# Optimization experiments

Hardware: AMD Instinct MI355X
Metric: run time of the kernel (lower is better)

The kernel has to match this reference:

```python
import jax, jax.numpy as jnp
import numpy as np
from jax import lax

RO = 4.0            # snake_config.ro (feature-map downsample ratio)
N_ADJ = 4           # snake_config.adj_num -> kernel = 2*4+1 = 9
K = 2 * N_ADJ + 1
DIL = (1, 1, 1, 2, 2, 4, 4)   # dilations of the 7 Snake residual circular convs
NMS_RADIUS = 2      # radius used in the iterative refinement cls_nms


def circ_conv(x, w, b, d):
    """Dilated circular conv along polygon axis. x:[N,C,P], w:[O,I,K]."""
    pad = N_ADJ * d
    xp = jnp.concatenate([x[..., -pad:], x, x[..., :pad]], axis=-1)
    y = lax.conv_general_dilated(xp, w, window_strides=(1,), padding='VALID',
                                 rhs_dilation=(d,),
                                 dimension_numbers=('NCH', 'OIH', 'NCH'))
    return y + b[None, :, None]


def conv1x1(x, w, b):
    # x:[N,C,P], w:[O,C] -> [N,O,P]
    return jnp.einsum('ncp,oc->nop', x, w) + b[None, :, None]


def bilinear_gather(cnn_feature, poly, ind):
    """grid_sample-style bilinear sampling (align_corners=False, zero pad).
    cnn_feature:[B,C,H,W], poly:[N,P,2] pixel coords, ind:[N] image index.
    Returns [N,C,P]."""
    B, C, H, W = cnn_feature.shape
    x = poly[..., 0] - 0.5
    y = poly[..., 1] - 0.5
    x0 = jnp.floor(x); y0 = jnp.floor(y)
    wx = x - x0; wy = y - y0
    x0i = x0.astype(jnp.int32); y0i = y0.astype(jnp.int32)

    def tap(yi, xi):
        valid = (xi >= 0) & (xi < W) & (yi >= 0) & (yi < H)
        xi_c = jnp.clip(xi, 0, W - 1)
        yi_c = jnp.clip(yi, 0, H - 1)
        f = cnn_feature[ind[:, None], :, yi_c, xi_c]  # [N,P,C]
        return f * valid[..., None]

    f00 = tap(y0i, x0i);     f01 = tap(y0i, x0i + 1)
    f10 = tap(y0i + 1, x0i); f11 = tap(y0i + 1, x0i + 1)
    out = (f00 * ((1 - wx) * (1 - wy))[..., None]
           + f01 * (wx * (1 - wy))[..., None]
           + f10 * ((1 - wx) * wy)[..., None]
           + f11 * (wx * wy)[..., None])
    return out.transpose(0, 2, 1)  # [N,C,P]


def cls_nms(cls, radius):
    """Circular local-max suppression of per-vertex scores. cls:[N,P,1]."""
    c = cls[..., 0]
    m = jnp.max(jnp.stack([jnp.roll(c, s, axis=1)
                           for s in range(-radius, radius + 1)], 0), axis=0)
    return jnp.where(c >= m, c, 0.0)[..., None]


def snake_body(x, head_w, head_b, res_w, res_b, fusion_w, fusion_b,
               pred1_w, pred1_b, pred2_w, pred2_b, pred3_w, pred3_b,
               cls1_w, cls1_b, cls2_w, cls2_b, cls3_w, cls3_b):
    h = jax.nn.relu(circ_conv(x, head_w, head_b, 1))
    states = [h]
    for i in range(7):  # fixed 7 residual layers, structurally distinct dilations
        r = jax.nn.relu(circ_conv(states[-1], res_w[i], res_b[i], DIL[i]))
        states.append(r + states[-1])
    state = jnp.concatenate(states, axis=1)                 # [N, 8*128, P]
    g = conv1x1(state, fusion_w, fusion_b)                  # [N, 256, P]
    g = jnp.max(g, axis=2, keepdims=True)
    g = jnp.broadcast_to(g, (state.shape[0], g.shape[1], state.shape[2]))
    state = jnp.concatenate([g, state], axis=1)             # [N, 1280, P]

    def head3(w1, b1, w2, b2, w3, b3):
        h1 = jax.nn.relu(conv1x1(state, w1, b1))
        h2 = jax.nn.relu(conv1x1(h1, w2, b2))
        return conv1x1(h2, w3, b3)

    offset = head3(pred1_w, pred1_b, pred2_w, pred2_b, pred3_w, pred3_b)  # [N,2,P]
    cls = head3(cls1_w, cls1_b, cls2_w, cls2_b, cls3_w, cls3_b)           # [N,1,P]
    return offset, cls


def setup_inputs() -> dict:
    key = jax.random.key(0)
    ks = jax.random.split(key, 32)
    B, C, H, W = 4, 64, 128, 128
    N, P = 512, 128
    SD = 128  # state_dim
    FD = 64 + 2 + 1  # feature_dim for iterative evolve_gcn
    std = 0.01  # conv init: normal(0, 0.01), bias 0 (matches module init)
    inp = {
        'cnn_feature': jax.random.normal(ks[0], (B, C, H, W), jnp.float32),
        'i_it_py': jax.random.uniform(ks[1], (N, P, 2), jnp.float32) * (W - 1),
        'c_it_py': jax.random.normal(ks[2], (N, P, 2), jnp.float32) * 0.2,
        'it_cls': jax.random.uniform(ks[3], (N, P), jnp.float32),
        'ind': jax.random.randint(ks[4], (N,), 0, B, jnp.int32),
        'head_w': jax.random.normal(ks[5], (SD, FD, K), jnp.float32) * std,
        'head_b': jnp.zeros((SD,), jnp.float32),
        'res_w': jax.random.normal(ks[6], (7, SD, SD, K), jnp.float32) * std,
        'res_b': jnp.zeros((7, SD), jnp.float32),
        'fusion_w': jax.random.normal(ks[7], (256, 8 * SD), jnp.float32) * std,
        'fusion_b': jnp.zeros((256,), jnp.float32),
        'pred1_w': jax.random.normal(ks[8], (256, 8 * SD + 256), jnp.float32) * std,
        'pred1_b': jnp.zeros((256,), jnp.float32),
        'pred2_w': jax.random.normal(ks[9], (64, 256), jnp.float32) * std,
        'pred2_b': jnp.zeros((64,), jnp.float32),
        'pred3_w': jax.random.normal(ks[10], (2, 64), jnp.float32) * std,
        'pred3_b': jnp.zeros((2,), jnp.float32),
        'cls1_w': jax.random.normal(ks[11], (256, 8 * SD + 256), jnp.float32) * std,
        'cls1_b': jnp.zeros((256,), jnp.float32),
        'cls2_w': jax.random.normal(ks[12], (64, 256), jnp.float32) * std,
        'cls2_b': jnp.zeros((64,), jnp.float32),
        'cls3_w': jax.random.normal(ks[13], (1, 64), jnp.float32) * std,
        'cls3_b': jnp.zeros((1,), jnp.float32),
    }
    return inp


def reference(cnn_feature, i_it_py, c_it_py, it_cls, ind,
              head_w, head_b, res_w, res_b, fusion_w, fusion_b,
              pred1_w, pred1_b, pred2_w, pred2_b, pred3_w, pred3_b,
              cls1_w, cls1_b, cls2_w, cls2_b, cls3_w, cls3_b):
    # evolve_poly: gather CNN features at vertices, concat scaled canonical
    # coords + per-vertex cls, run Snake, add offsets, NMS sigmoid scores.
    feat = bilinear_gather(cnn_feature, i_it_py, ind)        # [N,64,P]
    c = (c_it_py * RO).transpose(0, 2, 1)                    # [N,2,P]
    x = jnp.concatenate([feat, c, it_cls[:, None, :]], axis=1)  # [N,67,P]
    offset, cls = snake_body(x, head_w, head_b, res_w, res_b, fusion_w, fusion_b,
                             pred1_w, pred1_b, pred2_w, pred2_b, pred3_w, pred3_b,
                             cls1_w, cls1_b, cls2_w, cls2_b, cls3_w, cls3_b)
    i_poly = i_it_py * RO + offset.transpose(0, 2, 1)        # [N,P,2]
    cls = cls.transpose(0, 2, 1)                             # [N,P,1]
    nms = cls_nms(jax.nn.sigmoid(cls), NMS_RADIUS)           # [N,P,1]
    return i_poly, cls, nms
```

## Files before the change

kernel.cpp:

```cpp
#include <hip/hip_runtime.h>
#include <math.h>

typedef __attribute__((ext_vector_type(8))) short bf16x8;
typedef __attribute__((ext_vector_type(4))) float f32x4;

#define UOFF_CAW 0L
#define UOFF_FAW 2359296L
#define UOFF_H1W 2883584L
#define NB_TOT   3932160L
#define OFF_W1G  1966080L
#define OFF_W2S  2097152L
#define OFF_GRAW 2129920L
#define OFF_HG   2260992L
#define OFF_DYN  2523136L
#define REPACK_N 4096000L

__device__ inline ushort f2bf_rne(float x) {
  uint u = __float_as_uint(x);
  return (ushort)((u + 0x7FFFu + ((u >> 16) & 1u)) >> 16);
}
__device__ inline void split_bf(float x, ushort& h, ushort& l) {
  uint u = __float_as_uint(x);
  uint hb = (u + 0x7FFFu + ((u >> 16) & 1u)) & 0xFFFF0000u;
  h = (ushort)(hb >> 16);
  l = f2bf_rne(x - __uint_as_float(hb));
}
__device__ inline ushort bfsel(float w, int split) {
  uint u = __float_as_uint(w);
  uint hb = (u + 0x7FFFu + ((u >> 16) & 1u)) & 0xFFFF0000u;
  if (split == 0) return (ushort)(hb >> 16);
  float lo = w - __uint_as_float(hb);
  uint ul = __float_as_uint(lo);
  return (ushort)((ul + 0x7FFFu + ((ul >> 16) & 1u)) >> 16);
}
__device__ inline bf16x8 asb(uint4 a) {
  union { uint4 u; bf16x8 v; } x; x.u = a; return x.v;
}
__device__ inline f32x4 MFMA_(bf16x8 a, bf16x8 b, f32x4 c) {
  return __builtin_amdgcn_mfma_f32_16x16x32_bf16(a, b, c, 0, 0, 0);
}
__device__ inline uint2 pack2(ushort a, ushort b, ushort c, ushort d) {
  return make_uint2((uint)a | ((uint)b << 16), (uint)c | ((uint)d << 16));
}
__device__ inline void bar_lgkm() {
  asm volatile("s_waitcnt lgkmcnt(0)" ::: "memory");
  __builtin_amdgcn_s_barrier();
}

__device__ inline void read_frag_pair(const char* xb, int pc, int g, int ic,
                                      bf16x8& bh, bf16x8& bl) {
  const int s0 = (pc & 7) << 4;
  const char* a = xb + pc * 512 + (((ic * 64 + (g << 4))) ^ s0);
  bh = asb(*(const uint4*)a);
  bl = asb(*(const uint4*)(a + 256));
}

__global__ void k_repack(const float* __restrict__ head_w, const float* __restrict__ res_w,
                         const float* __restrict__ fusion_w,
                         const float* __restrict__ pred1_w, const float* __restrict__ cls1_w,
                         const float* __restrict__ pred2_w, const float* __restrict__ cls2_w,
                         float* __restrict__ ws) {
  const long j = (long)blockIdx.x * 256 + threadIdx.x;
  if (j >= REPACK_N) return;
  if (j < NB_TOT) {
    ushort* wsu = (ushort*)ws;
    float w;
    if (j < UOFF_FAW) {
      int e = (int)(j & 7); long q = j >> 3;
      int lane = (int)(q & 63); q >>= 6;
      int mt = (int)(q & 1); q >>= 1;
      int split = (int)(q & 1); q >>= 1;
      int ic = (int)(q & 3); q >>= 2;
      int tap = (int)(q % 9); q /= 9;
      int mp = (int)(q & 3); int l = (int)(q >> 2);
      int gg = lane >> 4;
      int kl = (e < 4) ? (4 * gg + e) : (16 + 4 * gg + e - 4);
      int m = mp * 32 + mt * 16 + (lane & 15);
      int i = ic * 32 + kl;
      if (l == 0) w = (i < 67) ? head_w[((long)m * 67 + i) * 9 + tap] : 0.f;
      else        w = res_w[(((long)(l - 1) * 128 + m) * 128 + i) * 9 + tap];
      wsu[j] = bfsel(w, split);
    } else if (j < UOFF_H1W) {
      long jj = j - UOFF_FAW;
      int e = (int)(jj & 7); long q = jj >> 3;
      int lane = (int)(q & 63); q >>= 6;
      int mt = (int)(q & 1); q >>= 1;
      int split = (int)(q & 1); q >>= 1;
      int ic = (int)(q & 3); q >>= 2;
      int fm2 = (int)(q & 7); int l = (int)(q >> 3);
      int gg = lane >> 4;
      int kl = (e < 4) ? (4 * gg + e) : (16 + 4 * gg + e - 4);
      int m = fm2 * 32 + mt * 16 + (lane & 15);
      int i = ic * 32 + kl;
      w = fusion_w[(long)m * 1024 + l * 128 + i];
      wsu[j] = bfsel(w, split);
    } else {
      long jj = j - UOFF_H1W;
      int e = (int)(jj & 7); long q = jj >> 3;
      int lane = (int)(q & 63); q >>= 6;
      int mt = (int)(q & 1); q >>= 1;
      int split = (int)(q & 1); q >>= 1;
      int ic = (int)(q & 3); q >>= 2;
      int slab = (int)(q & 7); q >>= 3;
      int mp = (int)(q & 7); int blk = (int)(q >> 3);
      int gg = lane >> 4;
      int kl = (e < 4) ? (4 * gg + e) : (16 + 4 * gg + e - 4);
      int m = blk * 256 + mp * 32 + mt * 16 + (lane & 15);
      int k = slab * 128 + ic * 32 + kl;
      w = (m < 256) ? pred1_w[(long)m * 1280 + 256 + k] : cls1_w[(long)(m - 256) * 1280 + 256 + k];
      wsu[j] = bfsel(w, split);
    }
  } else if (j < NB_TOT + 131072) {
    long q = j - NB_TOT; int o = (int)(q & 511); int c = (int)(q >> 9);
    ws[OFF_W1G + q] = (o < 256) ? pred1_w[(long)o * 1280 + c] : cls1_w[(long)(o - 256) * 1280 + c];
  } else {
    long q = j - NB_TOT - 131072;
    int o = (int)(q & 7); int i = (int)((q >> 3) & 255); int wvv = (int)(q >> 11);
    int jg = wvv * 8 + o;
    ws[OFF_W2S + q] = (jg < 64) ? pred2_w[jg * 256 + i] : cls2_w[(jg - 64) * 256 + i];
  }
}

__global__ __launch_bounds__(1024)
void k_conv(const float* __restrict__ cnn, const float* __restrict__ i_it,
            const float* __restrict__ c_it, const float* __restrict__ cls_in,
            const int* __restrict__ ind,
            const ushort* __restrict__ CAW, const ushort* __restrict__ FAW,
            const float* __restrict__ head_b, const float* __restrict__ res_b,
            float* __restrict__ graw, float* __restrict__ states, int p0) {
  __shared__ uint4 xt4[4096];
  __shared__ float scr[512];
  char* xb = (char*)xt4;
  const int ln = blockIdx.x, n = p0 + ln, t = threadIdx.x;
  const int lane = t & 63, li = lane & 15, g = lane >> 4;
  const int wv = __builtin_amdgcn_readfirstlane(t >> 6);
  const int mp = wv & 3, np = wv >> 2;
  const int fm2 = wv & 7, fq = wv >> 3;

  {
    const int p = t & 127, qg = t >> 7;
    const long nb = (long)n * 128 + p;
    const int sw = p & 7;
    float vals[4];
    if (qg < 4) {
      const float gx = i_it[nb * 2 + 0] - 0.5f;
      const float gy = i_it[nb * 2 + 1] - 0.5f;
      const float fx = floorf(gx), fy = floorf(gy);
      const float wx = gx - fx, wy = gy - fy;
      const int x0 = (int)fx, y0 = (int)fy, x1 = x0 + 1, y1 = y0 + 1;
      const bool vx0 = (x0 >= 0) & (x0 < 128), vx1 = (x1 >= 0) & (x1 < 128);
      const bool vy0 = (y0 >= 0) & (y0 < 128), vy1 = (y1 >= 0) & (y1 < 128);
      const int x0c = min(max(x0, 0), 127), x1c = min(max(x1, 0), 127);
      const int y0c = min(max(y0, 0), 127), y1c = min(max(y1, 0), 127);
      const float w00 = (vx0 && vy0) ? (1.f - wx) * (1.f - wy) : 0.f;
      const float w01 = (vx1 && vy0) ? wx * (1.f - wy) : 0.f;
      const float w10 = (vx0 && vy1) ? (1.f - wx) * wy : 0.f;
      const float w11 = (vx1 && vy1) ? wx * wy : 0.f;
      const long base = (long)ind[n] * (64L * 16384);
      const int a00 = y0c * 128 + x0c, a01 = y0c * 128 + x1c;
      const int a10 = y1c * 128 + x0c, a11 = y1c * 128 + x1c;
#pragma unroll
      for (int qq = 0; qq < 4; qq++) {
        ushort hh[4], ll[4];
#pragma unroll
        for (int cc = 0; cc < 4; cc++) {
          const int c = qg * 16 + qq * 4 + cc;
          const float* f = cnn + base + (long)c * 16384;
          float x = f[a00] * w00 + f[a01] * w01 + f[a10] * w10 + f[a11] * w11;
          split_bf(x, hh[cc], ll[cc]);
        }
        const int G = ((qg >> 1) * 4 + qq) ^ sw;
        char* a = xb + p * 512 + G * 16 + (qg & 1) * 8;
        *(uint2*)a = make_uint2((uint)hh[0] | ((uint)hh[1] << 16), (uint)hh[2] | ((uint)hh[3] << 16));
        *(uint2*)(a + 256) = make_uint2((uint)ll[0] | ((uint)ll[1] << 16), (uint)ll[2] | ((uint)ll[3] << 16));
      }
    } else {
      vals[0] = 0.f; vals[1] = 0.f; vals[2] = 0.f; vals[3] = 0.f;
#pragma unroll
      for (int qq = 0; qq < 4; qq++) {
        ushort hh[4], ll[4];
        if (qg == 4 && qq == 0) {
          float v0 = c_it[nb * 2 + 0] * 4.f, v1 = c_it[nb * 2 + 1] * 4.f, v2 = cls_in[nb];
          split_bf(v0, hh[0], ll[0]); split_bf(v1, hh[1], ll[1]); split_bf(v2, hh[2], ll[2]);
          hh[3] = 0; ll[3] = 0;
        } else {
          hh[0] = hh[1] = hh[2] = hh[3] = 0; ll[0] = ll[1] = ll[2] = ll[3] = 0;
        }
        const int G = ((qg >> 1) * 4 + qq) ^ sw;
        char* a = xb + p * 512 + G * 16 + (qg & 1) * 8;
        *(uint2*)a = make_uint2((uint)hh[0] | ((uint)hh[1] << 16), (uint)hh[2] | ((uint)hh[3] << 16));
        *(uint2*)(a + 256) = make_uint2((uint)ll[0] | ((uint)ll[1] << 16), (uint)ll[2] | ((uint)ll[3] << 16));
      }
    }
  }
  bar_lgkm();

  const f32x4 fz = {0.f, 0.f, 0.f, 0.f};
  f32x4 facc[2][4];
#pragma unroll
  for (int a = 0; a < 2; a++)
#pragma unroll
    for (int b = 0; b < 4; b++) facc[a][b] = fz;

  const uint4* caw = (const uint4*)CAW;
  const uint4* faw = (const uint4*)FAW;
  uint4* stq = (uint4*)(states + (long)ln * 131072);

  for (int l = 0; l < 8; l++) {
    const int dil = (l >= 6) ? 4 : ((l >= 4) ? 2 : 1);
    if (l > 0) {
      const int fl = l - 1;
#pragma unroll
      for (int k = 0; k < 4; k++) {
        uint4 tmp = xt4[k * 1024 + t];
        stq[fl * 4096 + k * 1024 + t] = tmp;
      }
      const uint4* fawl = faw + ((long)(fl * 8 + fm2)) * 1024 + lane;
#pragma unroll
      for (int ic = 0; ic < 4; ic++) {
        const uint4 ah0 = fawl[ic * 256 + 0];
        const uint4 ah1 = fawl[ic * 256 + 64];
        const uint4 al0 = fawl[ic * 256 + 128];
        const uint4 al1 = fawl[ic * 256 + 192];
        const bf16x8 Ah0 = asb(ah0), Ah1 = asb(ah1), Al0 = asb(al0), Al1 = asb(al1);
#pragma unroll
        for (int nt = 0; nt < 4; nt++) {
          const int pc = fq * 64 + nt * 16 + li;
          bf16x8 bh, bl;
          read_frag_pair(xb, pc, g, ic, bh, bl);
          facc[0][nt] = MFMA_(Ah0, bh, facc[0][nt]);
          facc[1][nt] = MFMA_(Ah1, bh, facc[1][nt]);
          facc[0][nt] = MFMA_(Ah0, bl, facc[0][nt]);
          facc[1][nt] = MFMA_(Ah1, bl, facc[1][nt]);
          facc[0][nt] = MFMA_(Al0, bh, facc[0][nt]);
          facc[1][nt] = MFMA_(Al1, bh, facc[1][nt]);
        }
      }
    }
    f32x4 cacc[2][2];
    cacc[0][0] = fz; cacc[0][1] = fz; cacc[1][0] = fz; cacc[1][1] = fz;
    const uint4* cawl = caw + ((long)(l * 4 + mp)) * 9216;
    for (int tap = 0; tap < 9; tap++) {
      const int shift = (tap - 4) * dil;
      const int pc0 = (np * 32 + li + shift + 128) & 127;
      const int pc1 = (np * 32 + 16 + li + shift + 128) & 127;
      const uint4* cawt = cawl + tap * 1024 + lane;
#pragma unroll
      for (int ic = 0; ic < 4; ic++) {
        bf16x8 bh0, bl0, bh1, bl1;
        read_frag_pair(xb, pc0, g, ic, bh0, bl0);
        read_frag_pair(xb, pc1, g, ic, bh1, bl1);
        const uint4 ah0 = cawt[ic * 256 + 0];
        const uint4 ah1 = cawt[ic * 256 + 64];
        const uint4 al0 = cawt[ic * 256 + 128];
        const uint4 al1 = cawt[ic * 256 + 192];
        const bf16x8 Ah0 = asb(ah0), Ah1 = asb(ah1), Al0 = asb(al0), Al1 = asb(al1);
        cacc[0][0] = MFMA_(Ah0, bh0, cacc[0][0]);
        cacc[0][1] = MFMA_(Ah0, bh1, cacc[0][1]);
        cacc[1][0] = MFMA_(Ah1, bh0, cacc[1][0]);
        cacc[1][1] = MFMA_(Ah1, bh1, cacc[1][1]);
        cacc[0][0] = MFMA_(Ah0, bl0, cacc[0][0]);
        cacc[0][1] = MFMA_(Ah0, bl1, cacc[0][1]);
        cacc[1][0] = MFMA_(Ah1, bl0, cacc[1][0]);
        cacc[1][1] = MFMA_(Ah1, bl1, cacc[1][1]);
        cacc[0][0] = MFMA_(Al0, bh0, cacc[0][0]);
        cacc[0][1] = MFMA_(Al0, bh1, cacc[0][1]);
        cacc[1][0] = MFMA_(Al1, bh0, cacc[1][0]);
        cacc[1][1] = MFMA_(Al1, bh1, cacc[1][1]);
      }
    }
    bar_lgkm();
    {
      const float* bsrc = (l == 0) ? head_b : (res_b + (l - 1) * 128);
#pragma unroll
      for (int mt = 0; mt < 2; mt++) {
        const float4 bias = *(const float4*)&bsrc[mp * 32 + mt * 16 + g * 4];
#pragma unroll
        for (int nt = 0; nt < 2; nt++) {
          const int p = np * 32 + nt * 16 + li;
          const int G = (mp * 4 + g) ^ (p & 7);
          char* a = xb + p * 512 + G * 16 + mt * 8;
          float v0 = fmaxf(cacc[mt][nt][0] + bias.x, 0.f);
          float v1 = fmaxf(cacc[mt][nt][1] + bias.y, 0.f);
          float v2 = fmaxf(cacc[mt][nt][2] + bias.z, 0.f);
          float v3 = fmaxf(cacc[mt][nt][3] + bias.w, 0.f);
          if (l > 0) {
            const uint2 oh = *(const uint2*)a;
            const uint2 ol = *(const uint2*)(a + 256);
            v0 += __uint_as_float((oh.x & 0xFFFFu) << 16) + __uint_as_float((ol.x & 0xFFFFu) << 16);
            v1 += __uint_as_float(oh.x & 0xFFFF0000u) + __uint_as_float(ol.x & 0xFFFF0000u);
            v2 += __uint_as_float((oh.y & 0xFFFFu) << 16) + __uint_as_float((ol.y & 0xFFFFu) << 16);
            v3 += __uint_as_float(oh.y & 0xFFFF0000u) + __uint_as_float(ol.y & 0xFFFF0000u);
          }
          ushort hh[4], ll[4];
          split_bf(v0, hh[0], ll[0]); split_bf(v1, hh[1], ll[1]);
          split_bf(v2, hh[2], ll[2]); split_bf(v3, hh[3], ll[3]);
          *(uint2*)a = make_uint2((uint)hh[0] | ((uint)hh[1] << 16), (uint)hh[2] | ((uint)hh[3] << 16));
          *(uint2*)(a + 256) = make_uint2((uint)ll[0] | ((uint)ll[1] << 16), (uint)ll[2] | ((uint)ll[3] << 16));
        }
      }
    }
    bar_lgkm();
  }

  {
#pragma unroll
    for (int k = 0; k < 4; k++) {
      uint4 tmp = xt4[k * 1024 + t];
      stq[7 * 4096 + k * 1024 + t] = tmp;
    }
    const uint4* fawl = faw + ((long)(7 * 8 + fm2)) * 1024 + lane;
#pragma unroll
    for (int ic = 0; ic < 4; ic++) {
      const uint4 ah0 = fawl[ic * 256 + 0];
      const uint4 ah1 = fawl[ic * 256 + 64];
      const uint4 al0 = fawl[ic * 256 + 128];
      const uint4 al1 = fawl[ic * 256 + 192];
      const bf16x8 Ah0 = asb(ah0), Ah1 = asb(ah1), Al0 = asb(al0), Al1 = asb(al1);
#pragma unroll
      for (int nt = 0; nt < 4; nt++) {
        const int pc = fq * 64 + nt * 16 + li;
        bf16x8 bh, bl;
        read_frag_pair(xb, pc, g, ic, bh, bl);
        facc[0][nt] = MFMA_(Ah0, bh, facc[0][nt]);
        facc[1][nt] = MFMA_(Ah1, bh, facc[1][nt]);
        facc[0][nt] = MFMA_(Ah0, bl, facc[0][nt]);
        facc[1][nt] = MFMA_(Ah1, bl, facc[1][nt]);
        facc[0][nt] = MFMA_(Al0, bh, facc[0][nt]);
        facc[1][nt] = MFMA_(Al1, bh, facc[1][nt]);
      }
    }
  }

#pragma unroll
  for (int mt = 0; mt < 2; mt++) {
#pragma unroll
    for (int r = 0; r < 4; r++) {
      float m = fmaxf(fmaxf(facc[mt][0][r], facc[mt][1][r]),
                      fmaxf(facc[mt][2][r], facc[mt][3][r]));
#pragma unroll
      for (int s = 1; s < 16; s <<= 1) m = fmaxf(m, __shfl_xor(m, s, 64));
      if (li == 0) scr[(fm2 * 32 + mt * 16 + g * 4 + r) * 2 + fq] = m;
    }
  }
  bar_lgkm();
  if (t < 256) graw[(long)n * 256 + t] = fmaxf(scr[2 * t], scr[2 * t + 1]);
}

__global__ __launch_bounds__(512)
void k_hg(const float* __restrict__ graw, const float* __restrict__ fus_b,
          const float* __restrict__ W1G, const float* __restrict__ p1b, const float* __restrict__ c1b,
          float* __restrict__ hg, int p0) {
  __shared__ float sg[256];
  const int n = p0 + blockIdx.x, t = threadIdx.x;
  if (t < 256) sg[t] = graw[(long)n * 256 + t] + fus_b[t];
  __syncthreads();
  float s = (t < 256) ? p1b[t] : c1b[t - 256];
  const float* w = W1G + t;
#pragma unroll 8
  for (int c = 0; c < 256; c++) s = fmaf(w[(long)c * 512], sg[c], s);
  hg[(long)n * 512 + t] = s;
}

__global__ __launch_bounds__(1024)
void k_h1(const float* __restrict__ states, const ushort* __restrict__ H1W,
          const float* __restrict__ hg, float* __restrict__ h1, int p0) {
  __shared__ uint4 xt4[4096];
  char* xb = (char*)xt4;
  const int b = blockIdx.x, ln = b >> 1, blk = b & 1, t = threadIdx.x;
  const int n = p0 + ln;
  const int lane = t & 63, li = lane & 15, g = lane >> 4;
  const int wv = __builtin_amdgcn_readfirstlane(t >> 6);
  const int mp = wv & 7, q = wv >> 3;
  const uint4* sp = (const uint4*)(states + (long)ln * 131072);
  const uint4* aw = (const uint4*)H1W;
  const f32x4 fz = {0.f, 0.f, 0.f, 0.f};
  f32x4 acc[2][4];
#pragma unroll
  for (int a = 0; a < 2; a++)
#pragma unroll
    for (int c = 0; c < 4; c++) acc[a][c] = fz;

  uint4 stg[4];
#pragma unroll
  for (int k = 0; k < 4; k++) stg[k] = sp[k * 1024 + t];

  for (int s = 0; s < 8; s++) {
#pragma unroll
    for (int k = 0; k < 4; k++) xt4[k * 1024 + t] = stg[k];
    bar_lgkm();
    if (s < 7) {
#pragma unroll
      for (int k = 0; k < 4; k++) stg[k] = sp[(s + 1) * 4096 + k * 1024 + t];
    }
    const uint4* awl = aw + (((long)(blk * 8 + mp)) * 8 + s) * 1024 + lane;
#pragma unroll
    for (int ic = 0; ic < 4; ic++) {
      const uint4 ah0 = awl[ic * 256 + 0];
      const uint4 ah1 = awl[ic * 256 + 64];
      const uint4 al0 = awl[ic * 256 + 128];
      const uint4 al1 = awl[ic * 256 + 192];
      const bf16x8 Ah0 = asb(ah0), Ah1 = asb(ah1), Al0 = asb(al0), Al1 = asb(al1);
#pragma unroll
      for (int nt = 0; nt < 4; nt++) {
        const int pc = q * 64 + nt * 16 + li;
        bf16x8 bh, bl;
        read_frag_pair(xb, pc, g, ic, bh, bl);
        acc[0][nt] = MFMA_(Ah0, bh, acc[0][nt]);
        acc[1][nt] = MFMA_(Ah1, bh, acc[1][nt]);
        acc[0][nt] = MFMA_(Ah0, bl, acc[0][nt]);
        acc[1][nt] = MFMA_(Ah1, bl, acc[1][nt]);
        acc[0][nt] = MFMA_(Al0, bh, acc[0][nt]);
        acc[1][nt] = MFMA_(Al1, bh, acc[1][nt]);
      }
    }
    bar_lgkm();
  }
  const float* hgp = hg + (long)n * 512;
  float* hb = h1 + (long)ln * 65536;
#pragma unroll
  for (int mt = 0; mt < 2; mt++) {
    const int ob = blk * 256 + mp * 32 + mt * 16 + g * 4;
    const float4 hq = *(const float4*)&hgp[ob];
#pragma unroll
    for (int nt = 0; nt < 4; nt++) {
      const int p = q * 64 + nt * 16 + li;
      float* d = hb + (long)ob * 128 + p;
      d[0]   = fmaxf(acc[mt][nt][0] + hq.x, 0.f);
      d[128] = fmaxf(acc[mt][nt][1] + hq.y, 0.f);
      d[256] = fmaxf(acc[mt][nt][2] + hq.z, 0.f);
      d[384] = fmaxf(acc[mt][nt][3] + hq.w, 0.f);
    }
  }
}

__global__ __launch_bounds__(1024) __attribute__((amdgpu_waves_per_eu(4)))
void k_tail(const float* __restrict__ h1, const float* __restrict__ W2S,
            const float* __restrict__ p2b, const float* __restrict__ c2b,
            const float* __restrict__ p3w, const float* __restrict__ p3b,
            const float* __restrict__ c3w, const float* __restrict__ c3b,
            const float* __restrict__ i_it, float* __restrict__ out, int p0) {
  __shared__ float h2[16384];
  __shared__ float xb[2048], xc[2048];
  const int ln = blockIdx.x, n = p0 + ln, t = threadIdx.x;
  const int po = t & 63;
  const int wv = __builtin_amdgcn_readfirstlane(t >> 6);
  const float* h1p = h1 + (long)ln * 65536;
  const float* wbase = W2S + (long)wv * 2048;
  float a0[8], a1[8];
#pragma unroll
  for (int jj = 0; jj < 8; jj++) { a0[jj] = 0.f; a1[jj] = 0.f; }
  for (int c = 0; c < 16; c++) {
    __syncthreads();
    ((float2*)xb)[t] = ((const float2*)(h1p + (long)c * 2048))[t];
    ((float2*)xc)[t] = ((const float2*)(h1p + 32768 + (long)c * 2048))[t];
    __syncthreads();
    const float* xp = (wv < 8) ? xb : xc;
    const float* wc = wbase + c * 128;
#pragma unroll 4
    for (int i = 0; i < 16; i++) {
      const float xv0 = xp[i * 128 + po];
      const float xv1 = xp[i * 128 + po + 64];
      const float* w = wc + i * 8;
#pragma unroll
      for (int jj = 0; jj < 8; jj++) {
        a0[jj] = fmaf(w[jj], xv0, a0[jj]);
        a1[jj] = fmaf(w[jj], xv1, a1[jj]);
      }
    }
  }
#pragma unroll
  for (int jj = 0; jj < 8; jj++) {
    const int j = wv * 8 + jj;
    const float bb = (j < 64) ? p2b[j] : c2b[j - 64];
    h2[j * 128 + po] = fmaxf(a0[jj] + bb, 0.f);
    h2[j * 128 + po + 64] = fmaxf(a1[jj] + bb, 0.f);
  }
  __syncthreads();

  float sig = 0.f;
  const int pp = t & 127;
  if (t < 128) {
    float o0v = p3b[0], o1v = p3b[1], cv = c3b[0];
    for (int j = 0; j < 64; j++) {
      const float hp = h2[j * 128 + pp];
      const float hc = h2[(64 + j) * 128 + pp];
      o0v = fmaf(p3w[j], hp, o0v);
      o1v = fmaf(p3w[64 + j], hp, o1v);
      cv = fmaf(c3w[j], hc, cv);
    }
    const long ip = ((long)n * 128 + pp) * 2;
    out[ip + 0] = i_it[ip + 0] * 4.f + o0v;
    out[ip + 1] = i_it[ip + 1] * 4.f + o1v;
    out[131072 + (long)n * 128 + pp] = cv;
    sig = 1.f / (1.f + expf(-cv));
  }
  __syncthreads();
  if (t < 128) xb[pp] = sig;
  __syncthreads();
  if (t < 128) {
    float m = xb[pp];
#pragma unroll
    for (int s = 1; s <= 2; s++) {
      m = fmaxf(m, xb[(pp + s) & 127]);
      m = fmaxf(m, xb[(pp + 128 - s) & 127]);
    }
    out[196608 + (long)n * 128 + pp] = (sig >= m) ? sig : 0.f;
  }
}

extern "C" void kernel_launch(void* const* d_in, const int* in_sizes, int n_in,
                              void* d_out, int out_size, void* d_ws, size_t ws_size,
                              hipStream_t stream) {
  const float* cnn      = (const float*)d_in[0];
// ... 49 lines not shown
```

Baseline: 1.128 ms.

## Remap wave tiles in conv and h1 kernels, skip zero input slab at layer 0

Reassigns the per-wave MFMA tiles in k_conv and k_h1. Each wave now covers four 16-row output fragments over fewer points, so each B fragment read from LDS feeds more MFMAs and the total LDS traffic drops. The circular conv loop now runs only three input-channel groups at layer 0, where the fourth group is zero padding. The fusion 1x1 conv is folded into the layer loop after each conv, and waves_per_eu hints are added. This trades more weight fragments held in registers per wave and a larger reduction scratch for less shared-memory traffic, with some risk to occupancy.

```diff
diff --git a/kernel.cpp b/kernel.cpp
--- a/kernel.cpp
+++ b/kernel.cpp
@@ -38,9 +38,6 @@
 }
 __device__ inline f32x4 MFMA_(bf16x8 a, bf16x8 b, f32x4 c) {
   return __builtin_amdgcn_mfma_f32_16x16x32_bf16(a, b, c, 0, 0, 0);
-}
-__device__ inline uint2 pack2(ushort a, ushort b, ushort c, ushort d) {
-  return make_uint2((uint)a | ((uint)b << 16), (uint)c | ((uint)d << 16));
 }
 __device__ inline void bar_lgkm() {
   asm volatile("s_waitcnt lgkmcnt(0)" ::: "memory");
@@ -121,7 +118,7 @@
   }
 }
 
-__global__ __launch_bounds__(1024)
+__global__ __launch_bounds__(1024) __attribute__((amdgpu_waves_per_eu(4)))
 void k_conv(const float* __restrict__ cnn, const float* __restrict__ i_it,
             const float* __restrict__ c_it, const float* __restrict__ cls_in,
             const int* __restrict__ ind,
@@ -129,19 +126,18 @@
             const float* __restrict__ head_b, const float* __restrict__ res_b,
             float* __restrict__ graw, float* __restrict__ states, int p0) {
   __shared__ uint4 xt4[4096];
-  __shared__ float scr[512];
+  __shared__ float scr[1024];
   char* xb = (char*)xt4;
   const int ln = blockIdx.x, n = p0 + ln, t = threadIdx.x;
   const int lane = t & 63, li = lane & 15, g = lane >> 4;
   const int wv = __builtin_amdgcn_readfirstlane(t >> 6);
-  const int mp = wv & 3, np = wv >> 2;
-  const int fm2 = wv & 7, fq = wv >> 3;
+  const int mw = wv & 1, nw = wv >> 1;
+  const int fm = wv & 3, fqw = wv >> 2;
 
   {
     const int p = t & 127, qg = t >> 7;
     const long nb = (long)n * 128 + p;
     const int sw = p & 7;
-    float vals[4];
     if (qg < 4) {
       const float gx = i_it[nb * 2 + 0] - 0.5f;
       const float gy = i_it[nb * 2 + 1] - 0.5f;
@@ -175,7 +171,6 @@
         *(uint2*)(a + 256) = make_uint2((uint)ll[0] | ((uint)ll[1] << 16), (uint)ll[2] | ((uint)ll[3] << 16));
       }
     } else {
-      vals[0] = 0.f; vals[1] = 0.f; vals[2] = 0.f; vals[3] = 0.f;
 #pragma unroll
       for (int qq = 0; qq < 4; qq++) {
         ushort hh[4], ll[4];
@@ -196,11 +191,9 @@
   bar_lgkm();
 
   const f32x4 fz = {0.f, 0.f, 0.f, 0.f};
-  f32x4 facc[2][4];
-#pragma unroll
-  for (int a = 0; a < 2; a++)
-#pragma unroll
-    for (int b = 0; b < 4; b++) facc[a][b] = fz;
+  f32x4 facc[4][2];
+#pragma unroll
+  for (int a = 0; a < 4; a++) { facc[a][0] = fz; facc[a][1] = fz; }
 
   const uint4* caw = (const uint4*)CAW;
   const uint4* faw = (const uint4*)FAW;
@@ -208,143 +201,127 @@
 
   for (int l = 0; l < 8; l++) {
     const int dil = (l >= 6) ? 4 : ((l >= 4) ? 2 : 1);
-    if (l > 0) {
-      const int fl = l - 1;
-#pragma unroll
-      for (int k = 0; k < 4; k++) {
-        uint4 tmp = xt4[k * 1024 + t];
-        stq[fl * 4096 + k * 1024 + t] = tmp;
-      }
-      const uint4* fawl = faw + ((long)(fl * 8 + fm2)) * 1024 + lane;
+    const int nic = (l == 0) ? 3 : 4;
+    f32x4 cacc[4];
+    cacc[0] = fz; cacc[1] = fz; cacc[2] = fz; cacc[3] = fz;
+    const uint4* cawl = caw + ((long)(l * 4 + mw * 2)) * 9216;
+    for (int tap = 0; tap < 9; tap++) {
+      const int shift = (tap - 4) * dil;
+      const int pc = (nw * 16 + li + shift + 128) & 127;
+      const uint4* wt = cawl + tap * 1024 + lane;
+      for (int ic = 0; ic < nic; ic++) {
+        bf16x8 bh, bl;
+        read_frag_pair(xb, pc, g, ic, bh, bl);
+        const uint4* w0 = wt + ic * 256;
+        const bf16x8 Ah0 = asb(w0[0]),          Ah1 = asb(w0[64]);
+        const bf16x8 Al0 = asb(w0[128]),        Al1 = asb(w0[192]);
+        const bf16x8 Ah2 = asb(w0[9216]),       Ah3 = asb(w0[9216 + 64]);
+        const bf16x8 Al2 = asb(w0[9216 + 128]), Al3 = asb(w0[9216 + 192]);
+        cacc[0] = MFMA_(Ah0, bh, cacc[0]);
+        cacc[1] = MFMA_(Ah1, bh, cacc[1]);
+        cacc[2] = MFMA_(Ah2, bh, cacc[2]);
+        cacc[3] = MFMA_(Ah3, bh, cacc[3]);
+        cacc[0] = MFMA_(Ah0, bl, cacc[0]);
+        cacc[1] = MFMA_(Ah1, bl, cacc[1]);
+        cacc[2] = MFMA_(Ah2, bl, cacc[2]);
+        cacc[3] = MFMA_(Ah3, bl, cacc[3]);
+        cacc[0] = MFMA_(Al0, bh, cacc[0]);
+        cacc[1] = MFMA_(Al1, bh, cacc[1]);
+        cacc[2] = MFMA_(Al2, bh, cacc[2]);
+        cacc[3] = MFMA_(Al3, bh, cacc[3]);
+      }
+    }
+    bar_lgkm();
+    {
+      const float* bsrc = (l == 0) ? head_b : (res_b + (l - 1) * 128);
+      const int p = nw * 16 + li;
+      const int sw = (p & 7) << 4;
+#pragma unroll
+      for (int j = 0; j < 2; j++) {
+        const int f0 = 2 * j, f1 = 2 * j + 1;
+        const float4 b0 = *(const float4*)&bsrc[mw * 64 + f0 * 16 + g * 4];
+        const float4 b1 = *(const float4*)&bsrc[mw * 64 + f1 * 16 + g * 4];
+        float v[8];
+        v[0] = fmaxf(cacc[f0][0] + b0.x, 0.f);
+        v[1] = fmaxf(cacc[f0][1] + b0.y, 0.f);
+        v[2] = fmaxf(cacc[f0][2] + b0.z, 0.f);
+        v[3] = fmaxf(cacc[f0][3] + b0.w, 0.f);
+        v[4] = fmaxf(cacc[f1][0] + b1.x, 0.f);
+        v[5] = fmaxf(cacc[f1][1] + b1.y, 0.f);
+        v[6] = fmaxf(cacc[f1][2] + b1.z, 0.f);
+        v[7] = fmaxf(cacc[f1][3] + b1.w, 0.f);
+        char* a = xb + p * 512 + ((((mw * 2 + j) * 4 + g) << 4) ^ sw);
+        if (l > 0) {
+          const uint4 oh = *(const uint4*)a;
+          const uint4 ol = *(const uint4*)(a + 256);
+          const uint hw[4] = {oh.x, oh.y, oh.z, oh.w};
+          const uint lw[4] = {ol.x, ol.y, ol.z, ol.w};
+#pragma unroll
+          for (int k = 0; k < 8; k++) {
+            const uint hh = (k & 1) ? (hw[k >> 1] & 0xFFFF0000u) : ((hw[k >> 1] & 0xFFFFu) << 16);
+            const uint ll = (k & 1) ? (lw[k >> 1] & 0xFFFF0000u) : ((lw[k >> 1] & 0xFFFFu) << 16);
+            v[k] += __uint_as_float(hh) + __uint_as_float(ll);
+          }
+        }
+        ushort hh[8], ll[8];
+#pragma unroll
+        for (int k = 0; k < 8; k++) split_bf(v[k], hh[k], ll[k]);
+        *(uint4*)a = make_uint4((uint)hh[0] | ((uint)hh[1] << 16), (uint)hh[2] | ((uint)hh[3] << 16),
+                                (uint)hh[4] | ((uint)hh[5] << 16), (uint)hh[6] | ((uint)hh[7] << 16));
+        *(uint4*)(a + 256) = make_uint4((uint)ll[0] | ((uint)ll[1] << 16), (uint)ll[2] | ((uint)ll[3] << 16),
+                                        (uint)ll[4] | ((uint)ll[5] << 16), (uint)ll[6] | ((uint)ll[7] << 16));
+      }
+    }
+    bar_lgkm();
+    {
+      uint4* dst = stq + (long)l * 4096;
+#pragma unroll
+      for (int k = 0; k < 4; k++) dst[k * 1024 + t] = xt4[k * 1024 + t];
+      const uint4* fawl = faw + ((long)(l * 8 + fm * 2)) * 1024 + lane;
 #pragma unroll
       for (int ic = 0; ic < 4; ic++) {
-        const uint4 ah0 = fawl[ic * 256 + 0];
-        const uint4 ah1 = fawl[ic * 256 + 64];
-        const uint4 al0 = fawl[ic * 256 + 128];
-        const uint4 al1 = fawl[ic * 256 + 192];
-        const bf16x8 Ah0 = asb(ah0), Ah1 = asb(ah1), Al0 = asb(al0), Al1 = asb(al1);
-#pragma unroll
-        for (int nt = 0; nt < 4; nt++) {
-          const int pc = fq * 64 + nt * 16 + li;
+        const uint4* w0 = fawl + ic * 256;
+        const bf16x8 Ah0 = asb(w0[0]),          Ah1 = asb(w0[64]);
+        const bf16x8 Al0 = asb(w0[128]),        Al1 = asb(w0[192]);
+        const bf16x8 Ah2 = asb(w0[1024]),       Ah3 = asb(w0[1024 + 64]);
+        const bf16x8 Al2 = asb(w0[1024 + 128]), Al3 = asb(w0[1024 + 192]);
+#pragma unroll
+        for (int nt = 0; nt < 2; nt++) {
+          const int pc = fqw * 32 + nt * 16 + li;
           bf16x8 bh, bl;
           read_frag_pair(xb, pc, g, ic, bh, bl);
           facc[0][nt] = MFMA_(Ah0, bh, facc[0][nt]);
           facc[1][nt] = MFMA_(Ah1, bh, facc[1][nt]);
+          facc[2][nt] = MFMA_(Ah2, bh, facc[2][nt]);
+          facc[3][nt] = MFMA_(Ah3, bh, facc[3][nt]);
           facc[0][nt] = MFMA_(Ah0, bl, facc[0][nt]);
           facc[1][nt] = MFMA_(Ah1, bl, facc[1][nt]);
+          facc[2][nt] = MFMA_(Ah2, bl, facc[2][nt]);
+          facc[3][nt] = MFMA_(Ah3, bl, facc[3][nt]);
           facc[0][nt] = MFMA_(Al0, bh, facc[0][nt]);
           facc[1][nt] = MFMA_(Al1, bh, facc[1][nt]);
+          facc[2][nt] = MFMA_(Al2, bh, facc[2][nt]);
+          facc[3][nt] = MFMA_(Al3, bh, facc[3][nt]);
         }
       }
     }
-    f32x4 cacc[2][2];
-    cacc[0][0] = fz; cacc[0][1] = fz; cacc[1][0] = fz; cacc[1][1] = fz;
-    const uint4* cawl = caw + ((long)(l * 4 + mp)) * 9216;
-    for (int tap = 0; tap < 9; tap++) {
-      const int shift = (tap - 4) * dil;
-      const int pc0 = (np * 32 + li + shift + 128) & 127;
-      const int pc1 = (np * 32 + 16 + li + shift + 128) & 127;
-      const uint4* cawt = cawl + tap * 1024 + lane;
-#pragma unroll
-      for (int ic = 0; ic < 4; ic++) {
-        bf16x8 bh0, bl0, bh1, bl1;
-        read_frag_pair(xb, pc0, g, ic, bh0, bl0);
-        read_frag_pair(xb, pc1, g, ic, bh1, bl1);
-        const uint4 ah0 = cawt[ic * 256 + 0];
-        const uint4 ah1 = cawt[ic * 256 + 64];
-        const uint4 al0 = cawt[ic * 256 + 128];
-        const uint4 al1 = cawt[ic * 256 + 192];
-        const bf16x8 Ah0 = asb(ah0), Ah1 = asb(ah1), Al0 = asb(al0), Al1 = asb(al1);
-        cacc[0][0] = MFMA_(Ah0, bh0, cacc[0][0]);
-        cacc[0][1] = MFMA_(Ah0, bh1, cacc[0][1]);
-        cacc[1][0] = MFMA_(Ah1, bh0, cacc[1][0]);
-        cacc[1][1] = MFMA_(Ah1, bh1, cacc[1][1]);
-        cacc[0][0] = MFMA_(Ah0, bl0, cacc[0][0]);
-        cacc[0][1] = MFMA_(Ah0, bl1, cacc[0][1]);
-        cacc[1][0] = MFMA_(Ah1, bl0, cacc[1][0]);
-        cacc[1][1] = MFMA_(Ah1, bl1, cacc[1][1]);
-        cacc[0][0] = MFMA_(Al0, bh0, cacc[0][0]);
-        cacc[0][1] = MFMA_(Al0, bh1, cacc[0][1]);
-        cacc[1][0] = MFMA_(Al1, bh0, cacc[1][0]);
-        cacc[1][1] = MFMA_(Al1, bh1, cacc[1][1]);
-      }
-    }
-    bar_lgkm();
-    {
-      const float* bsrc = (l == 0) ? head_b : (res_b + (l - 1) * 128);
-#pragma unroll
-      for (int mt = 0; mt < 2; mt++) {
-        const float4 bias = *(const float4*)&bsrc[mp * 32 + mt * 16 + g * 4];
-#pragma unroll
-        for (int nt = 0; nt < 2; nt++) {
-          const int p = np * 32 + nt * 16 + li;
-          const int G = (mp * 4 + g) ^ (p & 7);
-          char* a = xb + p * 512 + G * 16 + mt * 8;
-          float v0 = fmaxf(cacc[mt][nt][0] + bias.x, 0.f);
-          float v1 = fmaxf(cacc[mt][nt][1] + bias.y, 0.f);
-          float v2 = fmaxf(cacc[mt][nt][2] + bias.z, 0.f);
-          float v3 = fmaxf(cacc[mt][nt][3] + bias.w, 0.f);
-          if (l > 0) {
-            const uint2 oh = *(const uint2*)a;
-            const uint2 ol = *(const uint2*)(a + 256);
-            v0 += __uint_as_float((oh.x & 0xFFFFu) << 16) + __uint_as_float((ol.x & 0xFFFFu) << 16);
-            v1 += __uint_as_float(oh.x & 0xFFFF0000u) + __uint_as_float(ol.x & 0xFFFF0000u);
-            v2 += __uint_as_float((oh.y & 0xFFFFu) << 16) + __uint_as_float((ol.y & 0xFFFFu) << 16);
-            v3 += __uint_as_float(oh.y & 0xFFFF0000u) + __uint_as_float(ol.y & 0xFFFF0000u);
-          }
-          ushort hh[4], ll[4];
-          split_bf(v0, hh[0], ll[0]); split_bf(v1, hh[1], ll[1]);
-          split_bf(v2, hh[2], ll[2]); split_bf(v3, hh[3], ll[3]);
-          *(uint2*)a = make_uint2((uint)hh[0] | ((uint)hh[1] << 16), (uint)hh[2] | ((uint)hh[3] << 16));
-          *(uint2*)(a + 256) = make_uint2((uint)ll[0] | ((uint)ll[1] << 16), (uint)ll[2] | ((uint)ll[3] << 16));
-        }
-      }
-    }
-    bar_lgkm();
-  }
-
-  {
-#pragma unroll
-    for (int k = 0; k < 4; k++) {
-      uint4 tmp = xt4[k * 1024 + t];
-      stq[7 * 4096 + k * 1024 + t] = tmp;
-    }
-    const uint4* fawl = faw + ((long)(7 * 8 + fm2)) * 1024 + lane;
-#pragma unroll
-    for (int ic = 0; ic < 4; ic++) {
-      const uint4 ah0 = fawl[ic * 256 + 0];
-      const uint4 ah1 = fawl[ic * 256 + 64];
-      const uint4 al0 = fawl[ic * 256 + 128];
-      const uint4 al1 = fawl[ic * 256 + 192];
-      const bf16x8 Ah0 = asb(ah0), Ah1 = asb(ah1), Al0 = asb(al0), Al1 = asb(al1);
-#pragma unroll
-      for (int nt = 0; nt < 4; nt++) {
-        const int pc = fq * 64 + nt * 16 + li;
-        bf16x8 bh, bl;
-        read_frag_pair(xb, pc, g, ic, bh, bl);
-        facc[0][nt] = MFMA_(Ah0, bh, facc[0][nt]);
-        facc[1][nt] = MFMA_(Ah1, bh, facc[1][nt]);
-        facc[0][nt] = MFMA_(Ah0, bl, facc[0][nt]);
-        facc[1][nt] = MFMA_(Ah1, bl, facc[1][nt]);
-        facc[0][nt] = MFMA_(Al0, bh, facc[0][nt]);
-        facc[1][nt] = MFMA_(Al1, bh, facc[1][nt]);
-      }
-    }
-  }
-
-#pragma unroll
-  for (int mt = 0; mt < 2; mt++) {
+  }
+
+#pragma unroll
+  for (int f = 0; f < 4; f++) {
 #pragma unroll
     for (int r = 0; r < 4; r++) {
-      float m = fmaxf(fmaxf(facc[mt][0][r], facc[mt][1][r]),
-                      fmaxf(facc[mt][2][r], facc[mt][3][r]));
+      float m = fmaxf(facc[f][0][r], facc[f][1][r]);
 #pragma unroll
       for (int s = 1; s < 16; s <<= 1) m = fmaxf(m, __shfl_xor(m, s, 64));
-      if (li == 0) scr[(fm2 * 32 + mt * 16 + g * 4 + r) * 2 + fq] = m;
+      if (li == 0) scr[(fm * 64 + f * 16 + g * 4 + r) * 4 + fqw] = m;
     }
   }
   bar_lgkm();
-  if (t < 256) graw[(long)n * 256 + t] = fmaxf(scr[2 * t], scr[2 * t + 1]);
+  if (t < 256) {
+    const float* sc = scr + t * 4;
+    graw[(long)n * 256 + t] = fmaxf(fmaxf(sc[0], sc[1]), fmaxf(sc[2], sc[3]));
+  }
 }
 
 __global__ __launch_bounds__(512)
@@ -362,7 +339,7 @@
   hg[(long)n * 512 + t] = s;
 }
 
-__global__ __launch_bounds__(1024)
+__global__ __launch_bounds__(1024) __attribute__((amdgpu_waves_per_eu(4)))
 void k_h1(const float* __restrict__ states, const ushort* __restrict__ H1W,
           const float* __restrict__ hg, float* __restrict__ h1, int p0) {
   __shared__ uint4 xt4[4096];
@@ -371,15 +348,13 @@
   const int n = p0 + ln;
   const int lane = t & 63, li = lane & 15, g = lane >> 4;
   const int wv = __builtin_amdgcn_readfirstlane(t >> 6);
-  const int mp = wv & 7, q = wv >> 3;
+  const int mw = wv & 3, qw = wv >> 2;
   const uint4* sp = (const uint4*)(states + (long)ln * 131072);
   const uint4* aw = (const uint4*)H1W;
   const f32x4 fz = {0.f, 0.f, 0.f, 0.f};
-  f32x4 acc[2][4];
-#pragma unroll
-  for (int a = 0; a < 2; a++)
-#pragma unroll
-    for (int c = 0; c < 4; c++) acc[a][c] = fz;
+  f32x4 acc[4][2];
+#pragma unroll
+  for (int a = 0; a < 4; a++) { acc[a][0] = fz; acc[a][1] = fz; }
 
   uint4 stg[4];
 #pragma unroll
@@ -393,25 +368,31 @@
 #pragma unroll
       for (int k = 0; k < 4; k++) stg[k] = sp[(s + 1) * 4096 + k * 1024 + t];
     }
-    const uint4* awl = aw + (((long)(blk * 8 + mp)) * 8 + s) * 1024 + lane;
+    const uint4* awl = aw + (((long)(blk * 8 + mw * 2)) * 8 + s) * 1024 + lane;
 #pragma unroll
     for (int ic = 0; ic < 4; ic++) {
-      const uint4 ah0 = awl[ic * 256 + 0];
-      const uint4 ah1 = awl[ic * 256 + 64];
-      const uint4 al0 = awl[ic * 256 + 128];
-      const uint4 al1 = awl[ic * 256 + 192];
-      const bf16x8 Ah0 = asb(ah0), Ah1 = asb(ah1), Al0 = asb(al0), Al1 = asb(al1);
-#pragma unroll
-      for (int nt = 0; nt < 4; nt++) {
-        const int pc = q * 64 + nt * 16 + li;
+      const uint4* w0 = awl + ic * 256;
+      const bf16x8 Ah0 = asb(w0[0]),          Ah1 = asb(w0[64]);
+      const bf16x8 Al0 = asb(w0[128]),        Al1 = asb(w0[192]);
+      const bf16x8 Ah2 = asb(w0[8192]),       Ah3 = asb(w0[8192 + 64]);
+      const bf16x8 Al2 = asb(w0[8192 + 128]), Al3 = asb(w0[8192 + 192]);
+#pragma unroll
+      for (int nt = 0; nt < 2; nt++) {
+        const int pc = qw * 32 + nt * 16 + li;
         bf16x8 bh, bl;
         read_frag_pair(xb, pc, g, ic, bh, bl);
         acc[0][nt] = MFMA_(Ah0, bh, acc[0][nt]);
         acc[1][nt] = MFMA_(Ah1, bh, acc[1][nt]);
+        acc[2][nt] = MFMA_(Ah2, bh, acc[2][nt]);
+        acc[3][nt] = MFMA_(Ah3, bh, acc[3][nt]);
         acc[0][nt] = MFMA_(Ah0, bl, acc[0][nt]);
         acc[1][nt] = MFMA_(Ah1, bl, acc[1][nt]);
+        acc[2][nt] = MFMA_(Ah2, bl, acc[2][nt]);
+        acc[3][nt] = MFMA_(Ah3, bl, acc[3][nt]);
         acc[0][nt] = MFMA_(Al0, bh, acc[0][nt]);
         acc[1][nt] = MFMA_(Al1, bh, acc[1][nt]);
+        acc[2][nt] = MFMA_(Al2, bh, acc[2][nt]);
+        acc[3][nt] = MFMA_(Al3, bh, acc[3][nt]);
       }
     }
     bar_lgkm();
@@ -419,17 +400,17 @@
   const float* hgp = hg + (long)n * 512;
   float* hb = h1 + (long)ln * 65536;
 #pragma unroll
-  for (int mt = 0; mt < 2; mt++) {
-    const int ob = blk * 256 + mp * 32 + mt * 16 + g * 4;
+  for (int f = 0; f < 4; f++) {
+    const int ob = blk * 256 + mw * 64 + f * 16 + g * 4;
     const float4 hq = *(const float4*)&hgp[ob];
 #pragma unroll
-    for (int nt = 0; nt < 4; nt++) {
-      const int p = q * 64 + nt * 16 + li;
+    for (int nt = 0; nt < 2; nt++) {
+      const int p = qw * 32 + nt * 16 + li;
       float* d = hb + (long)ob * 128 + p;
-      d[0]   = fmaxf(acc[mt][nt][0] + hq.x, 0.f);
-      d[128] = fmaxf(acc[mt][nt][1] + hq.y, 0.f);
-      d[256] = fmaxf(acc[mt][nt][2] + hq.z, 0.f);
-      d[384] = fmaxf(acc[mt][nt][3] + hq.w, 0.f);
+      d[0]   = fmaxf(acc[f][nt][0] + hq.x, 0.f);
+      d[128] = fmaxf(acc[f][nt][1] + hq.y, 0.f);
+      d[256] = fmaxf(acc[f][nt][2] + hq.z, 0.f);
+      d[384] = fmaxf(acc[f][nt][3] + hq.w, 0.f);
     }
   }
 }
```

New measurement: 1.239 ms. 9.9% more time.

## Fuse state spill into conv epilogue, skip zero channel group, widen LDS stores

Applied to the files above, without the earlier changes.

The per-layer state write to global memory moves out of a separate LDS-readback loop and into the conv epilogue, which now writes each 16-byte bf16 hi/lo pack to both LDS and the states buffer. The epilogue is restructured to pack both m-tiles into single uint4 LDS reads and writes. Layer 0 skips the fourth input-channel group, which holds only zero padding. waves_per_eu(4) is added to k_conv and k_h1 to limit register use, and a couple of barriers become __syncthreads. The aim is to cut LDS traffic, redundant MFMAs and barrier overhead, at the cost of scattered global stores and possible register pressure.

```diff
diff --git a/kernel.cpp b/kernel.cpp
--- a/kernel.cpp
+++ b/kernel.cpp
@@ -38,9 +38,6 @@
 }
 __device__ inline f32x4 MFMA_(bf16x8 a, bf16x8 b, f32x4 c) {
   return __builtin_amdgcn_mfma_f32_16x16x32_bf16(a, b, c, 0, 0, 0);
-}
-__device__ inline uint2 pack2(ushort a, ushort b, ushort c, ushort d) {
-  return make_uint2((uint)a | ((uint)b << 16), (uint)c | ((uint)d << 16));
 }
 __device__ inline void bar_lgkm() {
   asm volatile("s_waitcnt lgkmcnt(0)" ::: "memory");
@@ -121,7 +118,7 @@
   }
 }
 
-__global__ __launch_bounds__(1024)
+__global__ __launch_bounds__(1024) __attribute__((amdgpu_waves_per_eu(4)))
 void k_conv(const float* __restrict__ cnn, const float* __restrict__ i_it,
             const float* __restrict__ c_it, const float* __restrict__ cls_in,
             const int* __restrict__ ind,
@@ -141,7 +138,6 @@
     const int p = t & 127, qg = t >> 7;
     const long nb = (long)n * 128 + p;
     const int sw = p & 7;
-    float vals[4];
     if (qg < 4) {
       const float gx = i_it[nb * 2 + 0] - 0.5f;
       const float gy = i_it[nb * 2 + 1] - 0.5f;
@@ -175,7 +171,6 @@
         *(uint2*)(a + 256) = make_uint2((uint)ll[0] | ((uint)ll[1] << 16), (uint)ll[2] | ((uint)ll[3] << 16));
       }
     } else {
-      vals[0] = 0.f; vals[1] = 0.f; vals[2] = 0.f; vals[3] = 0.f;
 #pragma unroll
       for (int qq = 0; qq < 4; qq++) {
         ushort hh[4], ll[4];
@@ -193,7 +188,7 @@
       }
     }
   }
-  bar_lgkm();
+  __syncthreads();
 
   const f32x4 fz = {0.f, 0.f, 0.f, 0.f};
   f32x4 facc[2][4];
@@ -208,21 +203,14 @@
 
   for (int l = 0; l < 8; l++) {
     const int dil = (l >= 6) ? 4 : ((l >= 4) ? 2 : 1);
+    const int nic = (l == 0) ? 3 : 4;
     if (l > 0) {
-      const int fl = l - 1;
-#pragma unroll
-      for (int k = 0; k < 4; k++) {
-        uint4 tmp = xt4[k * 1024 + t];
-        stq[fl * 4096 + k * 1024 + t] = tmp;
-      }
-      const uint4* fawl = faw + ((long)(fl * 8 + fm2)) * 1024 + lane;
+      const uint4* fawl = faw + ((long)((l - 1) * 8 + fm2)) * 1024 + lane;
 #pragma unroll
       for (int ic = 0; ic < 4; ic++) {
-        const uint4 ah0 = fawl[ic * 256 + 0];
-        const uint4 ah1 = fawl[ic * 256 + 64];
-        const uint4 al0 = fawl[ic * 256 + 128];
-        const uint4 al1 = fawl[ic * 256 + 192];
-        const bf16x8 Ah0 = asb(ah0), Ah1 = asb(ah1), Al0 = asb(al0), Al1 = asb(al1);
+        const uint4* w0 = fawl + ic * 256;
+        const bf16x8 Ah0 = asb(w0[0]),   Ah1 = asb(w0[64]);
+        const bf16x8 Al0 = asb(w0[128]), Al1 = asb(w0[192]);
 #pragma unroll
         for (int nt = 0; nt < 4; nt++) {
           const int pc = fq * 64 + nt * 16 + li;
@@ -245,16 +233,13 @@
       const int pc0 = (np * 32 + li + shift + 128) & 127;
       const int pc1 = (np * 32 + 16 + li + shift + 128) & 127;
       const uint4* cawt = cawl + tap * 1024 + lane;
-#pragma unroll
-      for (int ic = 0; ic < 4; ic++) {
+      for (int ic = 0; ic < nic; ic++) {
         bf16x8 bh0, bl0, bh1, bl1;
         read_frag_pair(xb, pc0, g, ic, bh0, bl0);
         read_frag_pair(xb, pc1, g, ic, bh1, bl1);
-        const uint4 ah0 = cawt[ic * 256 + 0];
-        const uint4 ah1 = cawt[ic * 256 + 64];
-        const uint4 al0 = cawt[ic * 256 + 128];
-        const uint4 al1 = cawt[ic * 256 + 192];
-        const bf16x8 Ah0 = asb(ah0), Ah1 = asb(ah1), Al0 = asb(al0), Al1 = asb(al1);
+        const uint4* w0 = cawt + ic * 256;
+        const bf16x8 Ah0 = asb(w0[0]),   Ah1 = asb(w0[64]);
+        const bf16x8 Al0 = asb(w0[128]), Al1 = asb(w0[192]);
         cacc[0][0] = MFMA_(Ah0, bh0, cacc[0][0]);
         cacc[0][1] = MFMA_(Ah0, bh1, cacc[0][1]);
         cacc[1][0] = MFMA_(Ah1, bh0, cacc[1][0]);
@@ -272,51 +257,58 @@
     bar_lgkm();
     {
       const float* bsrc = (l == 0) ? head_b : (res_b + (l - 1) * 128);
-#pragma unroll
-      for (int mt = 0; mt < 2; mt++) {
-        const float4 bias = *(const float4*)&bsrc[mp * 32 + mt * 16 + g * 4];
-#pragma unroll
-        for (int nt = 0; nt < 2; nt++) {
-          const int p = np * 32 + nt * 16 + li;
-          const int G = (mp * 4 + g) ^ (p & 7);
-          char* a = xb + p * 512 + G * 16 + mt * 8;
-          float v0 = fmaxf(cacc[mt][nt][0] + bias.x, 0.f);
-          float v1 = fmaxf(cacc[mt][nt][1] + bias.y, 0.f);
-          float v2 = fmaxf(cacc[mt][nt][2] + bias.z, 0.f);
-          float v3 = fmaxf(cacc[mt][nt][3] + bias.w, 0.f);
-          if (l > 0) {
-            const uint2 oh = *(const uint2*)a;
-            const uint2 ol = *(const uint2*)(a + 256);
-            v0 += __uint_as_float((oh.x & 0xFFFFu) << 16) + __uint_as_float((ol.x & 0xFFFFu) << 16);
-            v1 += __uint_as_float(oh.x & 0xFFFF0000u) + __uint_as_float(ol.x & 0xFFFF0000u);
-            v2 += __uint_as_float((oh.y & 0xFFFFu) << 16) + __uint_as_float((ol.y & 0xFFFFu) << 16);
-            v3 += __uint_as_float(oh.y & 0xFFFF0000u) + __uint_as_float(ol.y & 0xFFFF0000u);
+      const float4 b0 = *(const float4*)&bsrc[mp * 32 + g * 4];
+      const float4 b1 = *(const float4*)&bsrc[mp * 32 + 16 + g * 4];
+#pragma unroll
+      for (int nt = 0; nt < 2; nt++) {
+        const int p = np * 32 + nt * 16 + li;
+        const int X = (mp * 64 + g * 16) ^ ((p & 7) << 4);
+        char* a = xb + p * 512 + X;
+        float v[8];
+        v[0] = fmaxf(cacc[0][nt][0] + b0.x, 0.f);
+        v[1] = fmaxf(cacc[0][nt][1] + b0.y, 0.f);
+        v[2] = fmaxf(cacc[0][nt][2] + b0.z, 0.f);
+        v[3] = fmaxf(cacc[0][nt][3] + b0.w, 0.f);
+        v[4] = fmaxf(cacc[1][nt][0] + b1.x, 0.f);
+        v[5] = fmaxf(cacc[1][nt][1] + b1.y, 0.f);
+        v[6] = fmaxf(cacc[1][nt][2] + b1.z, 0.f);
+        v[7] = fmaxf(cacc[1][nt][3] + b1.w, 0.f);
+        if (l > 0) {
+          const uint4 oh = *(const uint4*)a;
+          const uint4 ol = *(const uint4*)(a + 256);
+          const uint hw[4] = {oh.x, oh.y, oh.z, oh.w};
+          const uint lw[4] = {ol.x, ol.y, ol.z, ol.w};
+#pragma unroll
+          for (int k = 0; k < 8; k++) {
+            const uint hh = (k & 1) ? (hw[k >> 1] & 0xFFFF0000u) : ((hw[k >> 1] & 0xFFFFu) << 16);
+            const uint ll = (k & 1) ? (lw[k >> 1] & 0xFFFF0000u) : ((lw[k >> 1] & 0xFFFFu) << 16);
+            v[k] += __uint_as_float(hh) + __uint_as_float(ll);
           }
-          ushort hh[4], ll[4];
-          split_bf(v0, hh[0], ll[0]); split_bf(v1, hh[1], ll[1]);
-          split_bf(v2, hh[2], ll[2]); split_bf(v3, hh[3], ll[3]);
-          *(uint2*)a = make_uint2((uint)hh[0] | ((uint)hh[1] << 16), (uint)hh[2] | ((uint)hh[3] << 16));
-          *(uint2*)(a + 256) = make_uint2((uint)ll[0] | ((uint)ll[1] << 16), (uint)ll[2] | ((uint)ll[3] << 16));
         }
-      }
-    }
-    bar_lgkm();
+        ushort hh[8], ll[8];
+#pragma unroll
+        for (int k = 0; k < 8; k++) split_bf(v[k], hh[k], ll[k]);
+        const uint4 phi = make_uint4((uint)hh[0] | ((uint)hh[1] << 16), (uint)hh[2] | ((uint)hh[3] << 16),
+                                     (uint)hh[4] | ((uint)hh[5] << 16), (uint)hh[6] | ((uint)hh[7] << 16));
+        const uint4 plo = make_uint4((uint)ll[0] | ((uint)ll[1] << 16), (uint)ll[2] | ((uint)ll[3] << 16),
+                                     (uint)ll[4] | ((uint)ll[5] << 16), (uint)ll[6] | ((uint)ll[7] << 16));
+        *(uint4*)a = phi;
+        *(uint4*)(a + 256) = plo;
+        uint4* sd = stq + (long)l * 4096 + p * 32 + (X >> 4);
+        sd[0] = phi;
+        sd[16] = plo;
+      }
+    }
+    __syncthreads();
   }
 
   {
-#pragma unroll
-    for (int k = 0; k < 4; k++) {
-      uint4 tmp = xt4[k * 1024 + t];
-      stq[7 * 4096 + k * 1024 + t] = tmp;
-    }
     const uint4* fawl = faw + ((long)(7 * 8 + fm2)) * 1024 + lane;
 #pragma unroll
     for (int ic = 0; ic < 4; ic++) {
-      const uint4 ah0 = fawl[ic * 256 + 0];
-      const uint4 ah1 = fawl[ic * 256 + 64];
-      const uint4 al0 = fawl[ic * 256 + 128];
-      const uint4 al1 = fawl[ic * 256 + 192];
-      const bf16x8 Ah0 = asb(ah0), Ah1 = asb(ah1), Al0 = asb(al0), Al1 = asb(al1);
+      const uint4* w0 = fawl + ic * 256;
+      const bf16x8 Ah0 = asb(w0[0]),   Ah1 = asb(w0[64]);
+      const bf16x8 Al0 = asb(w0[128]), Al1 = asb(w0[192]);
 #pragma unroll
       for (int nt = 0; nt < 4; nt++) {
         const int pc = fq * 64 + nt * 16 + li;
@@ -362,7 +354,7 @@
   hg[(long)n * 512 + t] = s;
 }
 
-__global__ __launch_bounds__(1024)
+__global__ __launch_bounds__(1024) __attribute__((amdgpu_waves_per_eu(4)))
 void k_h1(const float* __restrict__ states, const ushort* __restrict__ H1W,
           const float* __restrict__ hg, float* __restrict__ h1, int p0) {
   __shared__ uint4 xt4[4096];
@@ -371,7 +363,7 @@
   const int n = p0 + ln;
   const int lane = t & 63, li = lane & 15, g = lane >> 4;
   const int wv = __builtin_amdgcn_readfirstlane(t >> 6);
-  const int mp = wv & 7, q = wv >> 3;
+  const int mw = wv & 7, qw = wv >> 3;
   const uint4* sp = (const uint4*)(states + (long)ln * 131072);
   const uint4* aw = (const uint4*)H1W;
   const f32x4 fz = {0.f, 0.f, 0.f, 0.f};
@@ -393,17 +385,15 @@
 #pragma unroll
       for (int k = 0; k < 4; k++) stg[k] = sp[(s + 1) * 4096 + k * 1024 + t];
     }
-    const uint4* awl = aw + (((long)(blk * 8 + mp)) * 8 + s) * 1024 + lane;
+    const uint4* awl = aw + (((long)(blk * 8 + mw)) * 8 + s) * 1024 + lane;
 #pragma unroll
     for (int ic = 0; ic < 4; ic++) {
-      const uint4 ah0 = awl[ic * 256 + 0];
-      const uint4 ah1 = awl[ic * 256 + 64];
-      const uint4 al0 = awl[ic * 256 + 128];
-      const uint4 al1 = awl[ic * 256 + 192];
-      const bf16x8 Ah0 = asb(ah0), Ah1 = asb(ah1), Al0 = asb(al0), Al1 = asb(al1);
+      const uint4* w0 = awl + ic * 256;
+      const bf16x8 Ah0 = asb(w0[0]),   Ah1 = asb(w0[64]);
+      const bf16x8 Al0 = asb(w0[128]), Al1 = asb(w0[192]);
 #pragma unroll
       for (int nt = 0; nt < 4; nt++) {
-        const int pc = q * 64 + nt * 16 + li;
+        const int pc = qw * 64 + nt * 16 + li;
         bf16x8 bh, bl;
         read_frag_pair(xb, pc, g, ic, bh, bl);
         acc[0][nt] = MFMA_(Ah0, bh, acc[0][nt]);
@@ -420,11 +410,11 @@
   float* hb = h1 + (long)ln * 65536;
 #pragma unroll
   for (int mt = 0; mt < 2; mt++) {
-    const int ob = blk * 256 + mp * 32 + mt * 16 + g * 4;
+    const int ob = blk * 256 + mw * 32 + mt * 16 + g * 4;
     const float4 hq = *(const float4*)&hgp[ob];
 #pragma unroll
     for (int nt = 0; nt < 4; nt++) {
-      const int p = q * 64 + nt * 16 + li;
+      const int p = qw * 64 + nt * 16 + li;
       float* d = hb + (long)ob * 128 + p;
       d[0]   = fmaxf(acc[mt][nt][0] + hq.x, 0.f);
       d[128] = fmaxf(acc[mt][nt][1] + hq.y, 0.f);
```

Measured after the change: 1.100 ms. 2.4% less time.
